# Kernel tuning notes

Measured on AMD Instinct MI355X. Metric: run time of the kernel, lower is better.

The kernel has to match this reference:

```python
import jax, jax.numpy as jnp
import numpy as np

B, T, H = 2, 2048, 1024
NH, DK = 16, 64          # num_heads, head_dim (key)
VD, DV = 1024, 64        # value_dim, head_v_dim
LCTX, CD = 512, 768      # context length, cond_token_dim
DW, DA, DG, DVR = 64, 64, 128, 16  # lora ranks: decay, a, gate, v
EPS = DK * 1e-5          # GroupNorm eps = head_dim * norm_eps
LOGW_SCALE = -0.6065306597126334   # -exp(-0.5)

def _tshift(x):
    # token shift: out[t] = x[t-1], out[0] = 0
    return jnp.pad(x, ((0, 0), (1, 0), (0, 0)))[:, :-1]

def _forward(hidden_states, context, v_first, x_r, x_w, x_k, x_v, x_a, x_g,
             k_k, k_a, r_k, W_r, W_k, W_v, W_o, W_cond,
             wA, wB, wb, aA, aB, ab, gA, gB, vA, vB, vb, gn_w, gn_b):
    b, t, _ = hidden_states.shape
    # --- cross-attention context: project then linear-resample to length t (align_corners=True) ---
    ctx = context @ W_cond                                  # [B, Lctx, H]
    L = ctx.shape[1]
    pos = jnp.arange(t) * ((L - 1) / (t - 1))
    lo = jnp.floor(pos).astype(jnp.int32)
    hi = jnp.minimum(lo + 1, L - 1)
    f = (pos - lo)[None, :, None]
    ctx = ctx[:, lo] * (1.0 - f) + ctx[:, hi] * f            # [B, T, H]

    dx = _tshift(hidden_states) - hidden_states
    dc = _tshift(ctx) - ctx
    xr = hidden_states + dx * x_r
    xw = hidden_states + dx * x_w
    xa = hidden_states + dx * x_a
    xg = hidden_states + dx * x_g
    xk = ctx + dc * x_k   # key/value come from the (resampled) context: cross attention
    xv = ctx + dc * x_v

    r = xr @ W_r
    w = LOGW_SCALE * jax.nn.sigmoid(jnp.tanh(xw @ wA) @ wB + wb)   # log decay in (-0.6065, 0)
    k = xk @ W_k
    v = xv @ W_v
    # layer_idx != 0: lerp toward v_first with learned gate
    v = v + jax.nn.sigmoid((xv @ vA) @ vB + vb) * (v_first - v)
    a = jax.nn.sigmoid((xa @ aA) @ aB + ab)                         # in-context learning rate
    g = jax.nn.sigmoid(xg @ gA) @ gB                                 # output gate (no bias)

    kk = (k * k_k).reshape(b, t, NH, DK)
    kk = kk / jnp.maximum(jnp.linalg.norm(kk, axis=-1, keepdims=True), 1e-12)
    k = k * (1.0 + (a - 1.0) * k_a)

    rh = r.reshape(b, t, NH, DK)
    wh = w.reshape(b, t, NH, DK)
    kh = k.reshape(b, t, NH, DK)
    vh = v.reshape(b, t, NH, DV)
    ah = -kk
    bh = kk * a.reshape(b, t, NH, DK)

    # --- RWKV7 generalized delta rule recurrence: S[b,h,i(val),j(key)] ---
    def step(S, inp):
        r_t, w_t, k_t, v_t, a_t, b_t = inp
        sab = jnp.einsum('bhij,bhj,bhk->bhik', S, a_t, b_t)
        S = S * jnp.exp(w_t)[:, :, None, :] + sab + jnp.einsum('bhi,bhj->bhij', v_t, k_t)
        return S, jnp.einsum('bhij,bhj->bhi', S, r_t)

    tr = lambda x: jnp.swapaxes(x, 0, 1)  # [T,B,NH,D]
    S0 = jnp.zeros((b, NH, DV, DK), hidden_states.dtype)
    _, o = jax.lax.scan(step, S0, (tr(rh), tr(wh), tr(kh), tr(vh), tr(ah), tr(bh)))
    o = jnp.swapaxes(o, 0, 1)             # [B,T,NH,DV]

    # GroupNorm(num_groups=NH) over value_dim per token
    mu = o.mean(-1, keepdims=True)
    var = o.var(-1, keepdims=True)
    o = (o - mu) * jax.lax.rsqrt(var + EPS)
    o = o.reshape(b, t, VD) * gn_w + gn_b
    # r_k-weighted direct readout
    o = o + ((rh * kh * r_k).sum(-1, keepdims=True) * vh).reshape(b, t, VD)
    return (o * g) @ W_o

def setup_inputs():
    ki = iter(jax.random.split(jax.random.key(0), 48))
    def nrm(shape, s=1.0):
        return jax.random.normal(next(ki), shape, jnp.float32) * s
    def uni(shape):
        return jax.random.uniform(next(ki), shape, dtype=jnp.float32)
    return {
        'hidden_states': nrm((B, T, H)),
        'context': nrm((B, LCTX, CD)),
        'v_first': nrm((B, T, VD)),
        'x_r': uni((1, 1, H)), 'x_w': uni((1, 1, H)), 'x_k': uni((1, 1, H)),
        'x_v': uni((1, 1, H)), 'x_a': uni((1, 1, H)), 'x_g': uni((1, 1, H)),
        'k_k': jnp.full((H,), 0.85, jnp.float32),
        'k_a': jnp.ones((H,), jnp.float32),
        'r_k': nrm((NH, DK), 0.1),
        'W_r': nrm((H, H), 0.03), 'W_k': nrm((H, H), 0.03),
        'W_v': nrm((H, VD), 0.03), 'W_o': nrm((VD, H), 0.03),
        'W_cond': nrm((CD, H), 0.03),
        'wA': nrm((H, DW), 0.05), 'wB': nrm((DW, H), 0.05), 'wb': nrm((H,), 0.3) - 4.0,
        'aA': nrm((H, DA), 0.05), 'aB': nrm((DA, H), 0.05), 'ab': nrm((H,), 0.1),
        'gA': nrm((H, DG), 0.05), 'gB': nrm((DG, VD), 0.05),
        'vA': nrm((H, DVR), 0.05), 'vB': nrm((DVR, VD), 0.05),
        'vb': jnp.ones((VD,), jnp.float32),
        'gn_w': jnp.ones((VD,), jnp.float32), 'gn_b': jnp.zeros((VD,), jnp.float32),
    }

def reference(hidden_states, context, v_first, x_r, x_w, x_k, x_v, x_a, x_g, k_k, k_a, r_k, W_r, W_k, W_v, W_o, W_cond, wA, wB, wb, aA, aB, ab, gA, gB, vA, vB, vb, gn_w, gn_b):
    return _forward(hidden_states, context, v_first, x_r, x_w, x_k, x_v, x_a, x_g, k_k, k_a, r_k, W_r, W_k, W_v, W_o, W_cond, wA, wB, wb, aA, aB, ab, gA, gB, vA, vB, vb, gn_w, gn_b)
```

## Files before the change

kernel.cpp:

```cpp
#include <hip/hip_runtime.h>
#include <cstddef>
#include <cstdint>

#define T_ 2048
#define H_ 1024
#define NH_ 16
#define LCTX 512
#define NC 64
#define CL 32

typedef __attribute__((ext_vector_type(4))) float f4;
typedef __attribute__((ext_vector_type(4))) unsigned short u16x4;
typedef __attribute__((ext_vector_type(8))) short bf16x8;
typedef __attribute__((ext_vector_type(4))) float f32x4;

#define REP16(X) X(0) X(1) X(2) X(3) X(4) X(5) X(6) X(7) X(8) X(9) X(10) X(11) X(12) X(13) X(14) X(15)
#define REP8(X) X(0) X(1) X(2) X(3) X(4) X(5) X(6) X(7)
#define REP4(X) X(0) X(1) X(2) X(3)

__device__ __forceinline__ float sgm(float x) { return 1.0f / (1.0f + expf(-x)); }
__device__ __forceinline__ f4 f4splat(float v) { f4 r; r.x = v; r.y = v; r.z = v; r.w = v; return r; }
__device__ __forceinline__ float hsum4(f4 v) { return (v.x + v.y) + (v.z + v.w); }

__device__ __forceinline__ float rdlane(float v, int l) {
    return __uint_as_float(__builtin_amdgcn_readlane(__float_as_uint(v), l));
}

__device__ __forceinline__ unsigned short f2bf(float x) {
    unsigned u = __float_as_uint(x);
    u += 0x7FFFu + ((u >> 16) & 1u);
    return (unsigned short)(u >> 16);
}
__device__ __forceinline__ float bf2f(unsigned short h) {
    return __uint_as_float(((unsigned)h) << 16);
}

__device__ __forceinline__ void split1(float x, unsigned short& h, unsigned short& l) {
    unsigned u = __float_as_uint(x);
    h = (unsigned short)(u >> 16);
    float r = x - __uint_as_float(u & 0xFFFF0000u);
    l = (unsigned short)(__float_as_uint(r) >> 16);
}
__device__ __forceinline__ void split4(f4 v, u16x4& h, u16x4& l) {
    unsigned short hh, ll;
    split1(v.x, hh, ll); h.x = hh; l.x = ll;
    split1(v.y, hh, ll); h.y = hh; l.y = ll;
    split1(v.z, hh, ll); h.z = hh; l.z = ll;
    split1(v.w, hh, ll); h.w = hh; l.w = ll;
}

__device__ __forceinline__ size_t toff4(int row, int c4, int kpan) {
    const int j = c4 & 31;
    return ((size_t)(row >> 4) * kpan + (c4 >> 5)) * 512
         + ((j & 15) >> 2) * 128 + (row & 15) * 8 + ((j >> 4) << 2);
}
__device__ __forceinline__ size_t toff1(int row, int k, int kpan) {
    const int j = k & 31;
    return ((size_t)(row >> 4) * kpan + (k >> 5)) * 512
         + ((j & 15) >> 2) * 128 + (row & 15) * 8 + ((j >> 4) << 2) + (j & 3);
}

__device__ __forceinline__ void gload16(const void* g, void* l) {
    __builtin_amdgcn_global_load_lds(
        (const __attribute__((address_space(1))) unsigned int*)g,
        (__attribute__((address_space(3))) unsigned int*)l, 16, 0, 0);
}

struct WSeg { const float* W; unsigned short* Th; unsigned short* Tl;
              int K, N, kpan, tile0, tilesN; };
struct WAll { WSeg s[13]; };

__global__ __launch_bounds__(256) void wtrans_all(WAll all)
{
    const int bid = blockIdx.x;
    int si = 0;
    #pragma unroll
    for (int i = 1; i < 13; ++i) if (bid >= all.s[i].tile0) si = i;
    const WSeg sg = all.s[si];
    const int local = bid - sg.tile0;
    const int k0 = (local / sg.tilesN) * 32;
    const int n0 = (local % sg.tilesN) * 32;

    __shared__ float tile[32][33];
    const int t = threadIdx.x;
    const int r = t >> 3, c4 = (t & 7) * 4;
    f4 v = f4splat(0.0f);
    if (k0 + r < sg.K && n0 + c4 < sg.N)
        v = *(const f4*)(sg.W + (size_t)(k0 + r) * sg.N + n0 + c4);
    tile[r][c4 + 0] = v.x; tile[r][c4 + 1] = v.y;
    tile[r][c4 + 2] = v.z; tile[r][c4 + 3] = v.w;
    __syncthreads();
    {
        const int n = n0 + r;
        float x0 = tile[c4 + 0][r], x1 = tile[c4 + 1][r];
        float x2 = tile[c4 + 2][r], x3 = tile[c4 + 3][r];
        u16x4 hv, lv;
        hv.x = f2bf(x0); lv.x = f2bf(x0 - bf2f(hv.x));
        hv.y = f2bf(x1); lv.y = f2bf(x1 - bf2f(hv.y));
        hv.z = f2bf(x2); lv.z = f2bf(x2 - bf2f(hv.z));
        hv.w = f2bf(x3); lv.w = f2bf(x3 - bf2f(hv.w));
        const size_t off = toff4(n, k0 + c4, sg.kpan);
        *(u16x4*)(sg.Th + off) = hv;
        *(u16x4*)(sg.Tl + off) = lv;
    }
}

__global__ __launch_bounds__(256) void ctx_split(
    const float* __restrict__ X, unsigned short* __restrict__ H,
    unsigned short* __restrict__ L)
{
    const int gid = blockIdx.x * 256 + threadIdx.x;
    const int row = gid / 192;
    const int c4 = (gid - row * 192) * 4;
    f4 v = *(const f4*)(X + (size_t)row * 768 + c4);
    u16x4 h, l; split4(v, h, l);
    const size_t off = toff4(row, c4, 24);
    *(u16x4*)(H + off) = h; *(u16x4*)(L + off) = l;
}

__global__ __launch_bounds__(256) void hs_lerp4(
    const float* __restrict__ hs,
    const float* __restrict__ x_r, const float* __restrict__ x_w,
    const float* __restrict__ x_a, const float* __restrict__ x_g,
    unsigned short* __restrict__ xr_h, unsigned short* __restrict__ xr_l,
    unsigned short* __restrict__ xw_h, unsigned short* __restrict__ xw_l,
    unsigned short* __restrict__ xa_h, unsigned short* __restrict__ xa_l,
    unsigned short* __restrict__ xg_h, unsigned short* __restrict__ xg_l)
{
    const int gid = blockIdx.x * 256 + threadIdx.x;
    const int c4 = (gid & 255) * 4;
    const int row = gid >> 8;
    const int tt = row & (T_ - 1);
    const f4 cur = *(const f4*)(hs + (size_t)row * H_ + c4);
    f4 prev = f4splat(0.0f);
    if (tt) prev = *(const f4*)(hs + (size_t)(row - 1) * H_ + c4);
    const f4 d = prev - cur;
    const size_t off = toff4(row, c4, 32);
    u16x4 h, l;
    split4(cur + d * (*(const f4*)(x_r + c4)), h, l);
    *(u16x4*)(xr_h + off) = h; *(u16x4*)(xr_l + off) = l;
    split4(cur + d * (*(const f4*)(x_w + c4)), h, l);
    *(u16x4*)(xw_h + off) = h; *(u16x4*)(xw_l + off) = l;
    split4(cur + d * (*(const f4*)(x_a + c4)), h, l);
    *(u16x4*)(xa_h + off) = h; *(u16x4*)(xa_l + off) = l;
    split4(cur + d * (*(const f4*)(x_g + c4)), h, l);
    *(u16x4*)(xg_h + off) = h; *(u16x4*)(xg_l + off) = l;
}

__device__ __forceinline__ f4 ctx_sample(const float* __restrict__ cp, int b, int t, int c4) {
    const float scale = (float)(511.0 / 2047.0);
    float tf = (float)t * scale;
    int lo = (int)tf;
    float f = tf - (float)lo;
    int hi = lo + 1; if (hi > LCTX - 1) hi = LCTX - 1;
    f4 cl = *(const f4*)(cp + (size_t)(b * LCTX + lo) * 1024 + c4);
    f4 ch = *(const f4*)(cp + (size_t)(b * LCTX + hi) * 1024 + c4);
    return cl + (ch - cl) * f;
}

__global__ __launch_bounds__(256) void ctx_lerp2(
    const float* __restrict__ cp,
    const float* __restrict__ x_k, const float* __restrict__ x_v,
    unsigned short* __restrict__ xk_h, unsigned short* __restrict__ xk_l,
    unsigned short* __restrict__ xv_h, unsigned short* __restrict__ xv_l)
{
    const int gid = blockIdx.x * 256 + threadIdx.x;
    const int c4 = (gid & 255) * 4;
    const int row = gid >> 8;
    const int b = row >> 11;
    const int tt = row & (T_ - 1);
    const f4 cur = ctx_sample(cp, b, tt, c4);
    f4 prev = f4splat(0.0f);
    if (tt) prev = ctx_sample(cp, b, tt - 1, c4);
    const f4 d = prev - cur;
    const size_t off = toff4(row, c4, 32);
    u16x4 h, l;
    split4(cur + d * (*(const f4*)(x_k + c4)), h, l);
    *(u16x4*)(xk_h + off) = h; *(u16x4*)(xk_l + off) = l;
    split4(cur + d * (*(const f4*)(x_v + c4)), h, l);
    *(u16x4*)(xv_h + off) = h; *(u16x4*)(xv_l + off) = l;
}

struct GSeg {
    const unsigned short* ATh; const unsigned short* ATl;
    const unsigned short* BTh; const unsigned short* BTl;
    float* C; unsigned short* Ch; unsigned short* Cl;
    const float* bias; const float* aux1; const float* aux2;
    int K, N, kpanC, epi;
};
struct GBatch { GSeg s[4]; };

template <int OSPLIT>
__global__ __launch_bounds__(256, 2) void mgemm(GBatch gb, int M)
{
    __shared__ __align__(16) unsigned short Ah_[8 * 512];
    __shared__ __align__(16) unsigned short Al_[8 * 512];
    __shared__ __align__(16) unsigned short Bh_[4 * 512];
    __shared__ __align__(16) unsigned short Bl_[4 * 512];
    const GSeg G = gb.s[blockIdx.z];
    const int bn = blockIdx.y * 64;
    if (bn >= G.N) return;
    const int K = G.K;
    const int kpan = K >> 5;
    const int tid = threadIdx.x;
    const int lane = tid & 63;
    const int wave = tid >> 6;
    const int bm = blockIdx.x * 128;
    const int g = lane >> 4, rr = lane & 15;
    const int sA0 = wave, sA1 = wave + 4;

    f32x4 acc[4][2];
    #pragma unroll
    for (int mi = 0; mi < 4; ++mi)
        #pragma unroll
        for (int ni = 0; ni < 2; ++ni)
            acc[mi][ni] = (f32x4)(0.0f);

    const size_t aBase0 = (size_t)((bm >> 4) + sA0) * kpan * 512;
    const size_t aBase1 = (size_t)((bm >> 4) + sA1) * kpan * 512;
    const size_t bBase  = (size_t)((bn >> 4) + wave) * kpan * 512;

    for (int k0 = 0; k0 < K; k0 += 32) {
        const size_t kp = (size_t)(k0 >> 5) * 512 + (size_t)lane * 8;
        gload16(G.ATh + aBase0 + kp, &Ah_[sA0 * 512]);
        gload16(G.ATh + aBase1 + kp, &Ah_[sA1 * 512]);
        gload16(G.ATl + aBase0 + kp, &Al_[sA0 * 512]);
        gload16(G.ATl + aBase1 + kp, &Al_[sA1 * 512]);
        gload16(G.BTh + bBase + kp, &Bh_[wave * 512]);
        gload16(G.BTl + bBase + kp, &Bl_[wave * 512]);
        __syncthreads();
        bf16x8 a_h[4], a_l[4], b_h[2], b_l[2];
        #pragma unroll
        for (int mi = 0; mi < 4; ++mi) {
            const int s = (wave >> 1) * 4 + mi;
            a_h[mi] = *(const bf16x8*)&Ah_[s * 512 + g * 128 + rr * 8];
            a_l[mi] = *(const bf16x8*)&Al_[s * 512 + g * 128 + rr * 8];
        }
        #pragma unroll
        for (int ni = 0; ni < 2; ++ni) {
            const int s = (wave & 1) * 2 + ni;
            b_h[ni] = *(const bf16x8*)&Bh_[s * 512 + g * 128 + rr * 8];
            b_l[ni] = *(const bf16x8*)&Bl_[s * 512 + g * 128 + rr * 8];
        }
        #pragma unroll
        for (int mi = 0; mi < 4; ++mi)
            #pragma unroll
            for (int ni = 0; ni < 2; ++ni) {
                acc[mi][ni] = __builtin_amdgcn_mfma_f32_16x16x32_bf16(a_h[mi], b_h[ni], acc[mi][ni], 0, 0, 0);
                acc[mi][ni] = __builtin_amdgcn_mfma_f32_16x16x32_bf16(a_h[mi], b_l[ni], acc[mi][ni], 0, 0, 0);
                acc[mi][ni] = __builtin_amdgcn_mfma_f32_16x16x32_bf16(a_l[mi], b_h[ni], acc[mi][ni], 0, 0, 0);
            }
        __syncthreads();
    }
    const int wm = (wave >> 1) * 64;
    const int wn = (wave & 1) * 32;
    const int epi = G.epi;
    #pragma unroll
    for (int mi = 0; mi < 4; ++mi)
        #pragma unroll
        for (int ni = 0; ni < 2; ++ni)
            #pragma unroll
            for (int q = 0; q < 4; ++q) {
                const int grow = bm + wm + mi * 16 + g * 4 + q;
                const int gcol = bn + wn + ni * 16 + rr;
                float x = acc[mi][ni][q];
                if (epi == 1) x = -0.6065306597126334f * sgm(x + G.bias[gcol]);
                else if (epi == 2) x = sgm(x + G.bias[gcol]);
                else if (epi == 3) {
                    const size_t o3 = (size_t)grow * G.N + gcol;
                    float vt = G.aux1[o3];
                    x = vt + sgm(x + G.bias[gcol]) * (G.aux2[o3] - vt);
                }
                else if (epi == 4) x = tanhf(x);
                else if (epi == 5) x = sgm(x);
                if (OSPLIT) {
                    if (gcol < G.kpanC * 32) {
                        unsigned short hh, ll;
                        split1(x, hh, ll);
                        const size_t off = toff1(grow, gcol, G.kpanC);
                        G.Ch[off] = hh; G.Cl[off] = ll;
                    }
                } else {
                    G.C[(size_t)grow * G.N + gcol] = x;
                }
            }
}

__global__ __launch_bounds__(256) void prep_k(
    float* __restrict__ k, const float* __restrict__ a,
    const float* __restrict__ k_k, const float* __restrict__ k_a,
    float* __restrict__ kk)
{
    const int gid = blockIdx.x * 256 + threadIdx.x;
    const int j = gid & 63;
    const int h = (gid >> 6) & (NH_ - 1);
    const int ch = h * 64 + j;
    const float kv = k[gid];
    float kkv = kv * k_k[ch];
    float ss = kkv * kkv;
    #pragma unroll
    for (int m = 32; m; m >>= 1) ss += __shfl_xor(ss, m, 64);
    const float nrm = fmaxf(sqrtf(ss), 1e-12f);
    kk[gid] = kkv / nrm;
    const float av = a[gid];
    k[gid] = kv * (1.0f + (av - 1.0f) * k_a[ch]);
}

__global__ __launch_bounds__(256, 1) void chunk_AU(
    const float* __restrict__ w, const float* __restrict__ k,
    const float* __restrict__ v, const float* __restrict__ kk,
    const float* __restrict__ a,
    float* __restrict__ Pbuf, float* __restrict__ Ubuf)
{
    const int bid = blockIdx.x;
    const int c = bid & (NC - 1);
    const int bh = bid >> 6;
    const int b = bh >> 4, h = bh & (NH_ - 1);
    const int tid = threadIdx.x;
    const int wv_ = tid >> 6;
    const bool isU = wv_ >= 2;
    const int lane = tid & 63;
    const int row = (wv_ & 1) * 32 + (lane >> 1);
    const int cb = (lane & 1) * 32;
    __shared__ float ew_s[2][64], ah_s[2][64], bh_s[2][64], kh_s[2][64], vh_s[2][64];

#define DECL_X(i) f4 x##i = f4splat(0.0f);
    REP8(DECL_X)
#undef DECL_X
    if (!isU) {
        const int local = row - cb;
#define INIT_Q(i) \
        if (local == 4*i+0) x##i.x = 1.0f; \
        else if (local == 4*i+1) x##i.y = 1.0f; \
        else if (local == 4*i+2) x##i.z = 1.0f; \
        else if (local == 4*i+3) x##i.w = 1.0f;
        REP8(INIT_Q)
#undef INIT_Q
    }

    size_t idx = (((size_t)b * T_ + (size_t)c * CL) * NH_ + h) * 64 + lane;
    float wvv = 0, kkv = 0, av = 0, kv = 0, vvv = 0;
    if (wv_ == 0) { wvv = w[idx]; kkv = kk[idx]; av = a[idx]; }
    else if (wv_ == 1) { kv = k[idx]; vvv = v[idx]; }
    if (wv_ == 0) { ew_s[0][lane] = expf(wvv); ah_s[0][lane] = -kkv; bh_s[0][lane] = kkv * av; }
    else if (wv_ == 1) { kh_s[0][lane] = kv; vh_s[0][lane] = vvv; }
    idx += NH_ * 64;
    if (wv_ == 0) { wvv = w[idx]; kkv = kk[idx]; av = a[idx]; }
    else if (wv_ == 1) { kv = k[idx]; vvv = v[idx]; }
    __syncthreads();

    for (int t = 0; t < CL; ++t) {
        const int buf = t & 1;
        if (t + 1 < CL) {
            const int nb = buf ^ 1;
            if (wv_ == 0) { ew_s[nb][lane] = expf(wvv); ah_s[nb][lane] = -kkv; bh_s[nb][lane] = kkv * av; }
            else if (wv_ == 1) { kh_s[nb][lane] = kv; vh_s[nb][lane] = vvv; }
            if (t + 2 < CL) {
                idx += NH_ * 64;
                if (wv_ == 0) { wvv = w[idx]; kkv = kk[idx]; av = a[idx]; }
                else if (wv_ == 1) { kv = k[idx]; vvv = v[idx]; }
            }
        }
        const f4* A4 = (const f4*)&ah_s[buf][cb];
        f4 da0 = x0 * A4[0] + x2 * A4[2];
        f4 da1 = x1 * A4[1] + x3 * A4[3];
        da0 += x4 * A4[4] + x6 * A4[6];
        da1 += x5 * A4[5] + x7 * A4[7];
        const float Dp = hsum4(da0 + da1);
        const float D = Dp + __shfl_xor(Dp, 1, 64);
        const float vcur = vh_s[buf][row];
        const f4* E4 = (const f4*)&ew_s[buf][cb];
        const f4* B4 = (const f4*)&bh_s[buf][cb];
        const f4* K4 = (const f4*)&kh_s[buf][cb];
        if (!isU) {
#define UPDQ_(i) { x##i = x##i * E4[i] + D * B4[i]; }
            REP8(UPDQ_)
#undef UPDQ_
        } else {
#define UPDU_(i) { x##i = x##i * E4[i] + D * B4[i] + vcur * K4[i]; }
            REP8(UPDU_)
#undef UPDU_
        }
        __syncthreads();
    }
    float* Dst = (isU ? Ubuf : Pbuf)
               + (((size_t)bh * NC + c) * 64 + row) * 64 + cb;
#define ST_(i) ((f4*)Dst)[i] = x##i;
    REP8(ST_)
#undef ST_
}

__global__ __launch_bounds__(64) void chunk_scan(
    const float* __restrict__ Pbuf, float* __restrict__ USbuf)
{
    const int wg = (blockIdx.x & 7) * 64 + (blockIdx.x >> 3);
    const int bh = wg >> 4;
    const int rg = wg & 15;
    const int j = threadIdx.x;
    const int r0 = rg * 4;

    float a0 = 0, a1 = 0, a2 = 0, a3 = 0;
    float u0, u1, u2, u3;
    float pA[64], pB[64];

    const size_t base = (size_t)bh * NC * 4096;
    {
        const float* Pb = Pbuf + base + j;
        #pragma unroll
        for (int k2 = 0; k2 < 64; ++k2) pA[k2] = Pb[k2 * 64];
        const float* Ub = USbuf + base + r0 * 64 + j;
        u0 = Ub[0]; u1 = Ub[64]; u2 = Ub[128]; u3 = Ub[192];
    }

#define SCAN_STEP(PC, PN, c) { \
    float n0 = u0, n1 = u1, n2 = u2, n3 = u3; \
    float* Ub = USbuf + base + (size_t)(c) * 4096 + r0 * 64 + j; \
    Ub[0] = a0; Ub[64] = a1; Ub[128] = a2; Ub[192] = a3; \
    if ((c) + 1 < NC) { \
        const float* Un = USbuf + base + (size_t)((c) + 1) * 4096 + r0 * 64 + j; \
        u0 = Un[0]; u1 = Un[64]; u2 = Un[128]; u3 = Un[192]; \
        const float* Pn = Pbuf + base + (size_t)((c) + 1) * 4096 + j; \
        _Pragma("unroll") \
        for (int k2 = 0; k2 < 64; ++k2) PN[k2] = Pn[k2 * 64]; \
    } \
    _Pragma("unroll") \
    for (int k2 = 0; k2 < 64; ++k2) { \
        const float s0 = rdlane(a0, k2), s1 = rdlane(a1, k2); \
        const float s2 = rdlane(a2, k2), s3 = rdlane(a3, k2); \
        n0 += s0 * PC[k2]; n1 += s1 * PC[k2]; \
        n2 += s2 * PC[k2]; n3 += s3 * PC[k2]; \
    } \
    a0 = n0; a1 = n1; a2 = n2; a3 = n3; }

    for (int c = 0; c < NC; c += 2) {
        SCAN_STEP(pA, pB, c)
        SCAN_STEP(pB, pA, c + 1)
    }
#undef SCAN_STEP
}

__global__ __launch_bounds__(256, 1) void chunk_out(
    const float* __restrict__ r, const float* __restrict__ w,
    const float* __restrict__ k, const float* __restrict__ v,
    const float* __restrict__ kk, const float* __restrict__ a,
    const float* __restrict__ Scbuf, float* __restrict__ o)
{
    const int bid = blockIdx.x;
    const int c = bid & (NC - 1);
    const int bh = bid >> 6;
    const int b = bh >> 4, h = bh & (NH_ - 1);
    const int tid = threadIdx.x;
    const int wv_ = tid >> 6;
    const int lane = tid & 63;
    const int row = wv_ * 16 + (lane >> 2);
    const int cb = (lane & 3) * 16;
    __shared__ float ew_s[2][64], ah_s[2][64], bh_s[2][64], kh_s[2][64], rh_s[2][64], vh_s[2][64];

#define DECL_S(i) f4 s##i;
    REP4(DECL_S)
#undef DECL_S
    const f4* Srow = (const f4*)(Scbuf + (((size_t)bh * NC + c) * 64 + row) * 64 + cb);
#define LD_S(i) s##i = Srow[i];
    REP4(LD_S)
#undef LD_S

    size_t idx = (((size_t)b * T_ + (size_t)c * CL) * NH_ + h) * 64 + lane;
    size_t obase = (((size_t)b * T_ + (size_t)c * CL) * NH_ + h) * 64;
    float wvv = 0, kkv = 0, av = 0, kv = 0, rv = 0, vvv = 0;
    if (wv_ == 0) { wvv = w[idx]; kkv = kk[idx]; av = a[idx]; }
    else if (wv_ == 1) { kv = k[idx]; rv = r[idx]; }
    else if (wv_ == 2) { vvv = v[idx]; }
    if (wv_ == 0) { ew_s[0][lane] = expf(wvv); ah_s[0][lane] = -kkv; bh_s[0][lane] = kkv * av; }
    else if (wv_ == 1) { kh_s[0][lane] = kv; rh_s[0][lane] = rv; }
    else if (wv_ == 2) { vh_s[0][lane] = vvv; }
    idx += NH_ * 64;
    if (wv_ == 0) { wvv = w[idx]; kkv = kk[idx]; av = a[idx]; }
    else if (wv_ == 1) { kv = k[idx]; rv = r[idx]; }
    else if (wv_ == 2) { vvv = v[idx]; }
    __syncthreads();

    for (int t = 0; t < CL; ++t) {
        const int buf = t & 1;
        if (t + 1 < CL) {
            const int nb = buf ^ 1;
            if (wv_ == 0) { ew_s[nb][lane] = expf(wvv); ah_s[nb][lane] = -kkv; bh_s[nb][lane] = kkv * av; }
            else if (wv_ == 1) { kh_s[nb][lane] = kv; rh_s[nb][lane] = rv; }
            else if (wv_ == 2) { vh_s[nb][lane] = vvv; }
            if (t + 2 < CL) {
                idx += NH_ * 64;
                if (wv_ == 0) { wvv = w[idx]; kkv = kk[idx]; av = a[idx]; }
                else if (wv_ == 1) { kv = k[idx]; rv = r[idx]; }
                else if (wv_ == 2) { vvv = v[idx]; }
            }
        }
        const f4* A4 = (const f4*)&ah_s[buf][cb];
        f4 ua = (s0 * A4[0] + s1 * A4[1]) + (s2 * A4[2] + s3 * A4[3]);
        float p = hsum4(ua);
        p += __shfl_xor(p, 1, 64);
        p += __shfl_xor(p, 2, 64);
        const float sa = p;
        const float vcur = vh_s[buf][row];
        const f4* E4 = (const f4*)&ew_s[buf][cb];
        const f4* B4 = (const f4*)&bh_s[buf][cb];
        const f4* K4 = (const f4*)&kh_s[buf][cb];
        const f4* R4 = (const f4*)&rh_s[buf][cb];
        f4 oa = f4splat(0.0f);
#define UPDO_(i) { s##i = s##i * E4[i] + sa * B4[i] + vcur * K4[i]; oa += s##i * R4[i]; }
        REP4(UPDO_)
#undef UPDO_
        float ow = hsum4(oa);
        ow += __shfl_xor(ow, 1, 64);
        ow += __shfl_xor(ow, 2, 64);
        if ((lane & 3) == 0) o[obase + row] = ow;
        obase += NH_ * 64;
        __syncthreads();
    }
}

__global__ __launch_bounds__(256) void postproc(
    const float* __restrict__ o, const float* __restrict__ r, const float* __restrict__ k,
    const float* __restrict__ v, const float* __restrict__ g, const float* __restrict__ r_k,
    const float* __restrict__ gn_w, const float* __restrict__ gn_b,
    unsigned short* __restrict__ og_h, unsigned short* __restrict__ og_l)
{
    const int gid = blockIdx.x * 256 + threadIdx.x;
    const int i = gid & 63;
    const int h = (gid >> 6) & (NH_ - 1);
    const int ch = h * 64 + i;
    const float ov = o[gid];
    float s1 = ov, s2 = ov * ov;
    float term = r[gid] * k[gid] * r_k[ch];
    #pragma unroll
    for (int m = 32; m; m >>= 1) {
        s1 += __shfl_xor(s1, m, 64);
        s2 += __shfl_xor(s2, m, 64);
        term += __shfl_xor(term, m, 64);
    }
    const float mu = s1 * (1.0f / 64.0f);
    const float var = s2 * (1.0f / 64.0f) - mu * mu;
    const float on = (ov - mu) * rsqrtf(var + 6.4e-4f);
    const float outv = (on * gn_w[ch] + gn_b[ch] + term * v[gid]) * g[gid];
    unsigned short hh, ll;
    split1(outv, hh, ll);
    const int row = gid >> 10;
    const int col = gid & 1023;
    const size_t off = toff1(row, col, 32);
    og_h[off] = hh; og_l[off] = ll;
}

extern "C" void kernel_launch(void* const* d_in, const int* in_sizes, int n_in,
                              void* d_out, int out_size, void* d_ws, size_t ws_size,
                              hipStream_t stream)
{
    const float* hs      = (const float*)d_in[0];
    const float* context = (const float*)d_in[1];
    const float* v_first = (const float*)d_in[2];
    const float* x_r = (const float*)d_in[3];
    const float* x_w = (const float*)d_in[4];
    const float* x_k = (const float*)d_in[5];
    const float* x_v = (const float*)d_in[6];
    const float* x_a = (const float*)d_in[7];
    const float* x_g = (const float*)d_in[8];
    const float* k_k = (const float*)d_in[9];
    const float* k_a = (const float*)d_in[10];
    const float* r_k = (const float*)d_in[11];
    const float* W_r = (const float*)d_in[12];
    const float* W_k = (const float*)d_in[13];
    const float* W_v = (const float*)d_in[14];
    const float* W_o = (const float*)d_in[15];
    const float* W_cond = (const float*)d_in[16];
    const float* wA = (const float*)d_in[17];
    const float* wB = (const float*)d_in[18];
    const float* wb = (const float*)d_in[19];
    const float* aA = (const float*)d_in[20];
    const float* aB = (const float*)d_in[21];
    const float* ab = (const float*)d_in[22];
    const float* gA = (const float*)d_in[23];
    const float* gB = (const float*)d_in[24];
    const float* vA = (const float*)d_in[25];
    const float* vB = (const float*)d_in[26];
    const float* vb = (const float*)d_in[27];
    const float* gn_w = (const float*)d_in[28];
    const float* gn_b = (const float*)d_in[29];
    (void)in_sizes; (void)n_in; (void)out_size; (void)ws_size;

    float* ws = (float*)d_ws;
    float* cp    = ws;
    float* rbuf  = cp    + (1 << 20);
    float* kbuf  = rbuf  + (4 << 20);
    float* vtmp  = kbuf  + (4 << 20);
    float* wbuf  = vtmp  + (4 << 20);
    float* abuf  = wbuf  + (4 << 20);
    float* obuf  = abuf  + (4 << 20);
    float* kkbuf = obuf  + (4 << 20);
    float* gbuf  = kkbuf + (4 << 20);
    float* vbuf  = gbuf  + (4 << 20);
    float* Pbuf  = vbuf  + (4 << 20);
    float* Ubuf  = Pbuf  + (8 << 20);
    float* endf  = Ubuf  + (8 << 20);

    unsigned short* xr_h = (unsigned short*)obuf;  unsigned short* xr_l = xr_h + (4 << 20);
    unsigned short* xw_h = (unsigned short*)Pbuf;  unsigned short* xw_l = xw_h + (4 << 20);
    unsigned short* xa_h = (unsigned short*)Ubuf;  unsigned short* xa_l = xa_h + (4 << 20);
    unsigned short* xg_h = (unsigned short*)kkbuf; unsigned short* xg_l = xg_h + (4 << 20);
    unsigned short* xk_h = (unsigned short*)gbuf;  unsigned short* xk_l = xk_h + (4 << 20);
    unsigned short* xv_h = (unsigned short*)vbuf;  unsigned short* xv_l = xv_h + (4 << 20);
    unsigned short* og_h = (unsigned short*)wbuf;  unsigned short* og_l = og_h + (4 << 20);

    unsigned short* u = (unsigned short*)endf;
    unsigned short* ctx_h = u;  u += 786432;
    unsigned short* ctx_l = u;  u += 786432;
    unsigned short* w1h = u;    u += 262144;
    unsigned short* w1l = u;    u += 262144;
    unsigned short* a1h = u;    u += 262144;
    unsigned short* a1l = u;    u += 262144;
    unsigned short* g1h = u;    u += 524288;
    unsigned short* g1l = u;    u += 524288;
    unsigned short* v1h = u;    u += 131072;
    unsigned short* v1l = u;    u += 131072;
    unsigned short* condT_h = u; u += 786432;
    unsigned short* condT_l = u; u += 786432;
    unsigned short* rT_h = u;    u += 1048576;
    unsigned short* rT_l = u;    u += 1048576;
    unsigned short* kT_h = u;    u += 1048576;
    unsigned short* kT_l = u;    u += 1048576;
    unsigned short* vT_h = u;    u += 1048576;
    unsigned short* vT_l = u;    u += 1048576;
    unsigned short* oT_h = u;    u += 1048576;
    unsigned short* oT_l = u;    u += 1048576;
    unsigned short* waT_h = u;   u += 65536;
    unsigned short* waT_l = u;   u += 65536;
    unsigned short* wbT_h = u;   u += 65536;
    unsigned short* wbT_l = u;   u += 65536;
    unsigned short* aaT_h = u;   u += 65536;
    unsigned short* aaT_l = u;   u += 65536;
    unsigned short* abT_h = u;   u += 65536;
    unsigned short* abT_l = u;   u += 65536;
    unsigned short* gaT_h = u;   u += 131072;
    unsigned short* gaT_l = u;   u += 131072;
    unsigned short* gbT_h = u;   u += 131072;
    unsigned short* gbT_l = u;   u += 131072;
    unsigned short* vaT_h = u;   u += 65536;
    unsigned short* vaT_l = u;   u += 65536;
    unsigned short* vbT_h = u;   u += 32768;
    unsigned short* vbT_l = u;   u += 32768;

    const dim3 blk(256);
    {
        WAll all;
        auto seg = [](const float* W, unsigned short* Th, unsigned short* Tl,
                      int K, int N, int Kpad, int Npad, int tile0) {
            WSeg s; s.W = W; s.Th = Th; s.Tl = Tl; s.K = K; s.N = N;
            s.kpan = Kpad / 32; s.tile0 = tile0; s.tilesN = Npad / 32; return s;
        };
        int t0 = 0;
        all.s[0]  = seg(W_cond, condT_h, condT_l, 768, 1024, 768, 1024, t0);  t0 += 24 * 32;
        all.s[1]  = seg(W_r, rT_h, rT_l, 1024, 1024, 1024, 1024, t0);         t0 += 32 * 32;
        all.s[2]  = seg(W_k, kT_h, kT_l, 1024, 1024, 1024, 1024, t0);         t0 += 32 * 32;
        all.s[3]  = seg(W_v, vT_h, vT_l, 1024, 1024, 1024, 1024, t0);         t0 += 32 * 32;
        all.s[4]  = seg(W_o, oT_h, oT_l, 1024, 1024, 1024, 1024, t0);         t0 += 32 * 32;
        all.s[5]  = seg(wA, waT_h, waT_l, 1024, 64, 1024, 64, t0);            t0 += 32 * 2;
        all.s[6]  = seg(wB, wbT_h, wbT_l, 64, 1024, 64, 1024, t0);            t0 += 2 * 32;
        all.s[7]  = seg(aA, aaT_h, aaT_l, 1024, 64, 1024, 64, t0);            t0 += 32 * 2;
        all.s[8]  = seg(aB, abT_h, abT_l, 64, 1024, 64, 1024, t0);            t0 += 2 * 32;
        all.s[9]  = seg(gA, gaT_h, gaT_l, 1024, 128, 1024, 128, t0);          t0 += 32 * 4;
        all.s[10] = seg(gB, gbT_h, gbT_l, 128, 1024, 128, 1024, t0);          t0 += 4 * 32;
        all.s[11] = seg(vA, vaT_h, vaT_l, 1024, 16, 1024, 64, t0);            t0 += 32 * 2;
        all.s[12] = seg(vB, vbT_h, vbT_l, 16, 1024, 32, 1024, t0);            t0 += 1 * 32;
        wtrans_all<<<dim3(t0), blk, 0, stream>>>(all);
    }

    auto GS = [](const unsigned short* ah, const unsigned short* al,
                 const unsigned short* bh, const unsigned short* bl,
                 float* c, unsigned short* ch, unsigned short* cl,
                 int K, int N, int kpanC, int epi,
                 const float* bias, const float* a1, const float* a2) {
        GSeg s; s.ATh = ah; s.ATl = al; s.BTh = bh; s.BTl = bl;
        s.C = c; s.Ch = ch; s.Cl = cl; s.bias = bias; s.aux1 = a1; s.aux2 = a2;
        s.K = K; s.N = N; s.kpanC = kpanC; s.epi = epi; return s;
    };

    ctx_split<<<dim3(768), blk, 0, stream>>>(context, ctx_h, ctx_l);
    hs_lerp4<<<dim3(4096), blk, 0, stream>>>(hs, x_r, x_w, x_a, x_g,
                                             xr_h, xr_l, xw_h, xw_l, xa_h, xa_l, xg_h, xg_l);
    {
        GBatch gb;
        gb.s[0] = GS(ctx_h, ctx_l, condT_h, condT_l, cp, nullptr, nullptr,
                     768, 1024, 0, 0, nullptr, nullptr, nullptr);
        gb.s[1] = gb.s[0]; gb.s[2] = gb.s[0]; gb.s[3] = gb.s[0];
        mgemm<0><<<dim3(8, 16, 1), blk, 0, stream>>>(gb, 1024);
    }
    ctx_lerp2<<<dim3(4096), blk, 0, stream>>>(cp, x_k, x_v, xk_h, xk_l, xv_h, xv_l);

    {
        GBatch gb;
        gb.s[0] = GS(xr_h, xr_l, rT_h, rT_l, rbuf, nullptr, nullptr,
                     1024, 1024, 0, 0, nullptr, nullptr, nullptr);
        gb.s[1] = GS(xk_h, xk_l, kT_h, kT_l, kbuf, nullptr, nullptr,
                     1024, 1024, 0, 0, nullptr, nullptr, nullptr);
        gb.s[2] = GS(xv_h, xv_l, vT_h, vT_l, vtmp, nullptr, nullptr,
                     1024, 1024, 0, 0, nullptr, nullptr, nullptr);
        gb.s[3] = gb.s[0];
        mgemm<0><<<dim3(32, 16, 3), blk, 0, stream>>>(gb, 4096);
    }
    {
        GBatch gb;
        gb.s[0] = GS(xw_h, xw_l, waT_h, waT_l, nullptr, w1h, w1l,
                     1024, 64, 2, 4, nullptr, nullptr, nullptr);
        gb.s[1] = GS(xa_h, xa_l, aaT_h, aaT_l, nullptr, a1h, a1l,
                     1024, 64, 2, 0, nullptr, nullptr, nullptr);
        gb.s[2] = GS(xg_h, xg_l, gaT_h, gaT_l, nullptr, g1h, g1l,
                     1024, 128, 4, 5, nullptr, nullptr, nullptr);
        gb.s[3] = GS(xv_h, xv_l, vaT_h, vaT_l, nullptr, v1h, v1l,
                     1024, 64, 1, 0, nullptr, nullptr, nullptr);
        mgemm<1><<<dim3(32, 2, 4), blk, 0, stream>>>(gb, 4096);
    }
    {
        GBatch gb;
        gb.s[0] = GS(w1h, w1l, wbT_h, wbT_l, wbuf, nullptr, nullptr,
                     64, 1024, 0, 1, wb, nullptr, nullptr);
        gb.s[1] = GS(a1h, a1l, abT_h, abT_l, abuf, nullptr, nullptr,
                     64, 1024, 0, 2, ab, nullptr, nullptr);
        gb.s[2] = GS(g1h, g1l, gbT_h, gbT_l, gbuf, nullptr, nullptr,
                     128, 1024, 0, 0, nullptr, nullptr, nullptr);
        gb.s[3] = GS(v1h, v1l, vbT_h, vbT_l, vbuf, nullptr, nullptr,
                     32, 1024, 0, 3, vb, vtmp, v_first);
        mgemm<0><<<dim3(32, 16, 4), blk, 0, stream>>>(gb, 4096);
    }

    prep_k<<<dim3(16384), blk, 0, stream>>>(kbuf, abuf, k_k, k_a, kkbuf);
    chunk_AU<<<dim3(2048), dim3(256), 0, stream>>>(wbuf, kbuf, vbuf, kkbuf, abuf, Pbuf, Ubuf);
    chunk_scan<<<dim3(512), dim3(64), 0, stream>>>(Pbuf, Ubuf);
    chunk_out<<<dim3(2048), dim3(256), 0, stream>>>(rbuf, wbuf, kbuf, vbuf, kkbuf, abuf, Ubuf, obuf);

    postproc<<<dim3(16384), blk, 0, stream>>>(obuf, rbuf, kbuf, vbuf, gbuf, r_k, gn_w, gn_b, og_h, og_l);
    {
        GBatch gb;
        gb.s[0] = GS(og_h, og_l, oT_h, oT_l, (float*)d_out, nullptr, nullptr,
                     1024, 1024, 0, 0, nullptr, nullptr, nullptr);
        gb.s[1] = gb.s[0]; gb.s[2] = gb.s[0]; gb.s[3] = gb.s[0];
        mgemm<0><<<dim3(32, 16, 1), blk, 0, stream>>>(gb, 4096);
    }
}
```

Baseline: 635.9 us.

## Map each chunk to one wavefront with per-lane state rows and readlane broadcasts

chunk_AU and chunk_out now give each (batch, head, chunk) a single 64-lane wavefront instead of a 256-thread block. Each lane holds a full 64-column state row in registers, and per-timestep vectors are broadcast with readlane instead of being staged through double-buffered shared memory behind __syncthreads. This removes the shared-memory traffic and block barriers and packs four chunks per block, so the grids shrink by four. In exchange each lane keeps 128 floats (chunk_AU) or 64 floats (chunk_out) live, which raises register pressure and can cause spills, and each step issues many readlane instructions.

```diff
diff --git a/kernel.cpp b/kernel.cpp
--- a/kernel.cpp
+++ b/kernel.cpp
@@ -13,10 +13,6 @@
 typedef __attribute__((ext_vector_type(4))) unsigned short u16x4;
 typedef __attribute__((ext_vector_type(8))) short bf16x8;
 typedef __attribute__((ext_vector_type(4))) float f32x4;
-
-#define REP16(X) X(0) X(1) X(2) X(3) X(4) X(5) X(6) X(7) X(8) X(9) X(10) X(11) X(12) X(13) X(14) X(15)
-#define REP8(X) X(0) X(1) X(2) X(3) X(4) X(5) X(6) X(7)
-#define REP4(X) X(0) X(1) X(2) X(3)
 
 __device__ __forceinline__ float sgm(float x) { return 1.0f / (1.0f + expf(-x)); }
 __device__ __forceinline__ f4 f4splat(float v) { f4 r; r.x = v; r.y = v; r.z = v; r.w = v; return r; }
@@ -306,88 +302,69 @@
     k[gid] = kv * (1.0f + (av - 1.0f) * k_a[ch]);
 }
 
-__global__ __launch_bounds__(256, 1) void chunk_AU(
+__global__ __launch_bounds__(256) void chunk_AU(
     const float* __restrict__ w, const float* __restrict__ k,
     const float* __restrict__ v, const float* __restrict__ kk,
     const float* __restrict__ a,
     float* __restrict__ Pbuf, float* __restrict__ Ubuf)
 {
-    const int bid = blockIdx.x;
-    const int c = bid & (NC - 1);
-    const int bh = bid >> 6;
+    const int gw = blockIdx.x * 4 + (threadIdx.x >> 6);
+    const int c = gw & (NC - 1);
+    const int bh = gw >> 6;
     const int b = bh >> 4, h = bh & (NH_ - 1);
-    const int tid = threadIdx.x;
-    const int wv_ = tid >> 6;
-    const bool isU = wv_ >= 2;
-    const int lane = tid & 63;
-    const int row = (wv_ & 1) * 32 + (lane >> 1);
-    const int cb = (lane & 1) * 32;
-    __shared__ float ew_s[2][64], ah_s[2][64], bh_s[2][64], kh_s[2][64], vh_s[2][64];
-
-#define DECL_X(i) f4 x##i = f4splat(0.0f);
-    REP8(DECL_X)
-#undef DECL_X
-    if (!isU) {
-        const int local = row - cb;
-#define INIT_Q(i) \
-        if (local == 4*i+0) x##i.x = 1.0f; \
-        else if (local == 4*i+1) x##i.y = 1.0f; \
-        else if (local == 4*i+2) x##i.z = 1.0f; \
-        else if (local == 4*i+3) x##i.w = 1.0f;
-        REP8(INIT_Q)
-#undef INIT_Q
-    }
+    const int lane = threadIdx.x & 63;
+
+    float q[64], uu[64];
+    #pragma unroll
+    for (int j = 0; j < 64; ++j) { q[j] = (j == lane) ? 1.0f : 0.0f; uu[j] = 0.0f; }
 
     size_t idx = (((size_t)b * T_ + (size_t)c * CL) * NH_ + h) * 64 + lane;
-    float wvv = 0, kkv = 0, av = 0, kv = 0, vvv = 0;
-    if (wv_ == 0) { wvv = w[idx]; kkv = kk[idx]; av = a[idx]; }
-    else if (wv_ == 1) { kv = k[idx]; vvv = v[idx]; }
-    if (wv_ == 0) { ew_s[0][lane] = expf(wvv); ah_s[0][lane] = -kkv; bh_s[0][lane] = kkv * av; }
-    else if (wv_ == 1) { kh_s[0][lane] = kv; vh_s[0][lane] = vvv; }
-    idx += NH_ * 64;
-    if (wv_ == 0) { wvv = w[idx]; kkv = kk[idx]; av = a[idx]; }
-    else if (wv_ == 1) { kv = k[idx]; vvv = v[idx]; }
-    __syncthreads();
+    float wv = w[idx], kkv = kk[idx], av = a[idx], kv = k[idx], vv = v[idx];
 
     for (int t = 0; t < CL; ++t) {
-        const int buf = t & 1;
+        const float e_own = expf(wv);
+        const float ah_own = -kkv;
+        const float bh_own = kkv * av;
+        const float k_own = kv;
+        const float v_own = vv;
         if (t + 1 < CL) {
-            const int nb = buf ^ 1;
-            if (wv_ == 0) { ew_s[nb][lane] = expf(wvv); ah_s[nb][lane] = -kkv; bh_s[nb][lane] = kkv * av; }
-            else if (wv_ == 1) { kh_s[nb][lane] = kv; vh_s[nb][lane] = vvv; }
-            if (t + 2 < CL) {
-                idx += NH_ * 64;
-                if (wv_ == 0) { wvv = w[idx]; kkv = kk[idx]; av = a[idx]; }
-                else if (wv_ == 1) { kv = k[idx]; vvv = v[idx]; }
-            }
+            idx += NH_ * 64;
+            wv = w[idx]; kkv = kk[idx]; av = a[idx]; kv = k[idx]; vv = v[idx];
         }
-        const f4* A4 = (const f4*)&ah_s[buf][cb];
-        f4 da0 = x0 * A4[0] + x2 * A4[2];
-        f4 da1 = x1 * A4[1] + x3 * A4[3];
-        da0 += x4 * A4[4] + x6 * A4[6];
-        da1 += x5 * A4[5] + x7 * A4[7];
-        const float Dp = hsum4(da0 + da1);
-        const float D = Dp + __shfl_xor(Dp, 1, 64);
-        const float vcur = vh_s[buf][row];
-        const f4* E4 = (const f4*)&ew_s[buf][cb];
-        const f4* B4 = (const f4*)&bh_s[buf][cb];
-        const f4* K4 = (const f4*)&kh_s[buf][cb];
-        if (!isU) {
-#define UPDQ_(i) { x##i = x##i * E4[i] + D * B4[i]; }
-            REP8(UPDQ_)
-#undef UPDQ_
-        } else {
-#define UPDU_(i) { x##i = x##i * E4[i] + D * B4[i] + vcur * K4[i]; }
-            REP8(UPDU_)
-#undef UPDU_
+        float dq0 = 0, dq1 = 0, dq2 = 0, dq3 = 0;
+        float du0 = 0, du1 = 0, du2 = 0, du3 = 0;
+        #pragma unroll
+        for (int j = 0; j < 64; j += 4) {
+            const float a0 = rdlane(ah_own, j);
+            const float a1 = rdlane(ah_own, j + 1);
+            const float a2 = rdlane(ah_own, j + 2);
+            const float a3 = rdlane(ah_own, j + 3);
+            dq0 += q[j] * a0;     dq1 += q[j + 1] * a1;
+            dq2 += q[j + 2] * a2; dq3 += q[j + 3] * a3;
+            du0 += uu[j] * a0;     du1 += uu[j + 1] * a1;
+            du2 += uu[j + 2] * a2; du3 += uu[j + 3] * a3;
         }
-        __syncthreads();
-    }
-    float* Dst = (isU ? Ubuf : Pbuf)
-               + (((size_t)bh * NC + c) * 64 + row) * 64 + cb;
-#define ST_(i) ((f4*)Dst)[i] = x##i;
-    REP8(ST_)
-#undef ST_
+        const float Dq = (dq0 + dq1) + (dq2 + dq3);
+        const float Du = (du0 + du1) + (du2 + du3);
+        #pragma unroll
+        for (int j = 0; j < 64; ++j) {
+            const float ej = rdlane(e_own, j);
+            const float bj = rdlane(bh_own, j);
+            const float kj = rdlane(k_own, j);
+            q[j]  = q[j]  * ej + Dq * bj;
+            uu[j] = uu[j] * ej + Du * bj + v_own * kj;
+        }
+    }
+    float* Pd = Pbuf + (((size_t)bh * NC + c) * 64 + lane) * 64;
+    float* Ud = Ubuf + (((size_t)bh * NC + c) * 64 + lane) * 64;
+    #pragma unroll
+    for (int jj = 0; jj < 16; ++jj) {
+        f4 tp, tu;
+        tp.x = q[4 * jj];  tp.y = q[4 * jj + 1];  tp.z = q[4 * jj + 2];  tp.w = q[4 * jj + 3];
+        tu.x = uu[4 * jj]; tu.y = uu[4 * jj + 1]; tu.z = uu[4 * jj + 2]; tu.w = uu[4 * jj + 3];
+        *(f4*)(Pd + 4 * jj) = tp;
+        *(f4*)(Ud + 4 * jj) = tu;
+    }
 }
 
 __global__ __launch_bounds__(64) void chunk_scan(
@@ -439,81 +416,75 @@
 #undef SCAN_STEP
 }
 
-__global__ __launch_bounds__(256, 1) void chunk_out(
+__global__ __launch_bounds__(256) void chunk_out(
     const float* __restrict__ r, const float* __restrict__ w,
     const float* __restrict__ k, const float* __restrict__ v,
     const float* __restrict__ kk, const float* __restrict__ a,
     const float* __restrict__ Scbuf, float* __restrict__ o)
 {
-    const int bid = blockIdx.x;
-    const int c = bid & (NC - 1);
-    const int bh = bid >> 6;
+    const int gw = blockIdx.x * 4 + (threadIdx.x >> 6);
+    const int c = gw & (NC - 1);
+    const int bh = gw >> 6;
     const int b = bh >> 4, h = bh & (NH_ - 1);
-    const int tid = threadIdx.x;
-    const int wv_ = tid >> 6;
-    const int lane = tid & 63;
-    const int row = wv_ * 16 + (lane >> 2);
-    const int cb = (lane & 3) * 16;
-    __shared__ float ew_s[2][64], ah_s[2][64], bh_s[2][64], kh_s[2][64], rh_s[2][64], vh_s[2][64];
-
-#define DECL_S(i) f4 s##i;
-    REP4(DECL_S)
-#undef DECL_S
-    const f4* Srow = (const f4*)(Scbuf + (((size_t)bh * NC + c) * 64 + row) * 64 + cb);
-#define LD_S(i) s##i = Srow[i];
-    REP4(LD_S)
-#undef LD_S
+    const int lane = threadIdx.x & 63;
+
+    float s[64];
+    {
+        const float* Srow = Scbuf + (((size_t)bh * NC + c) * 64 + lane) * 64;
+        #pragma unroll
+        for (int j = 0; j < 64; ++j) s[j] = Srow[j];
+    }
 
     size_t idx = (((size_t)b * T_ + (size_t)c * CL) * NH_ + h) * 64 + lane;
     size_t obase = (((size_t)b * T_ + (size_t)c * CL) * NH_ + h) * 64;
-    float wvv = 0, kkv = 0, av = 0, kv = 0, rv = 0, vvv = 0;
-    if (wv_ == 0) { wvv = w[idx]; kkv = kk[idx]; av = a[idx]; }
-    else if (wv_ == 1) { kv = k[idx]; rv = r[idx]; }
-    else if (wv_ == 2) { vvv = v[idx]; }
-    if (wv_ == 0) { ew_s[0][lane] = expf(wvv); ah_s[0][lane] = -kkv; bh_s[0][lane] = kkv * av; }
-    else if (wv_ == 1) { kh_s[0][lane] = kv; rh_s[0][lane] = rv; }
-    else if (wv_ == 2) { vh_s[0][lane] = vvv; }
-    idx += NH_ * 64;
-    if (wv_ == 0) { wvv = w[idx]; kkv = kk[idx]; av = a[idx]; }
-    else if (wv_ == 1) { kv = k[idx]; rv = r[idx]; }
-    else if (wv_ == 2) { vvv = v[idx]; }
-    __syncthreads();
+    float wv = w[idx], kkv = kk[idx], av = a[idx], kv = k[idx], rv = r[idx], vv = v[idx];
 
     for (int t = 0; t < CL; ++t) {
-        const int buf = t & 1;
+        const float e_own = expf(wv);
+        const float ah_own = -kkv;
+        const float bh_own = kkv * av;
+        const float k_own = kv;
+        const float r_own = rv;
+        const float v_own = vv;
         if (t + 1 < CL) {
-            const int nb = buf ^ 1;
-            if (wv_ == 0) { ew_s[nb][lane] = expf(wvv); ah_s[nb][lane] = -kkv; bh_s[nb][lane] = kkv * av; }
-            else if (wv_ == 1) { kh_s[nb][lane] = kv; rh_s[nb][lane] = rv; }
-            else if (wv_ == 2) { vh_s[nb][lane] = vvv; }
-            if (t + 2 < CL) {
-                idx += NH_ * 64;
-                if (wv_ == 0) { wvv = w[idx]; kkv = kk[idx]; av = a[idx]; }
-                else if (wv_ == 1) { kv = k[idx]; rv = r[idx]; }
-                else if (wv_ == 2) { vvv = v[idx]; }
+            idx += NH_ * 64;
+            wv = w[idx]; kkv = kk[idx]; av = a[idx]; kv = k[idx]; rv = r[idx]; vv = v[idx];
+        }
+        float d0 = 0, d1 = 0, d2 = 0, d3 = 0;
+        #pragma unroll
+        for (int j = 0; j < 64; j += 4) {
+            d0 += s[j]     * rdlane(ah_own, j);
+            d1 += s[j + 1] * rdlane(ah_own, j + 1);
+            d2 += s[j + 2] * rdlane(ah_own, j + 2);
+            d3 += s[j + 3] * rdlane(ah_own, j + 3);
+        }
+        const float sa = (d0 + d1) + (d2 + d3);
+        float o0 = 0, o1 = 0, o2 = 0, o3 = 0;
+        #pragma unroll
+        for (int j = 0; j < 64; j += 4) {
+            {
+                const float ej = rdlane(e_own, j), bj = rdlane(bh_own, j);
+                const float kj = rdlane(k_own, j), rj = rdlane(r_own, j);
+                s[j] = s[j] * ej + sa * bj + v_own * kj; o0 += s[j] * rj;
+            }
+            {
+                const float ej = rdlane(e_own, j + 1), bj = rdlane(bh_own, j + 1);
+                const float kj = rdlane(k_own, j + 1), rj = rdlane(r_own, j + 1);
+                s[j + 1] = s[j + 1] * ej + sa * bj + v_own * kj; o1 += s[j + 1] * rj;
+            }
+            {
+                const float ej = rdlane(e_own, j + 2), bj = rdlane(bh_own, j + 2);
+                const float kj = rdlane(k_own, j + 2), rj = rdlane(r_own, j + 2);
+                s[j + 2] = s[j + 2] * ej + sa * bj + v_own * kj; o2 += s[j + 2] * rj;
+            }
+            {
+                const float ej = rdlane(e_own, j + 3), bj = rdlane(bh_own, j + 3);
+                const float kj = rdlane(k_own, j + 3), rj = rdlane(r_own, j + 3);
+                s[j + 3] = s[j + 3] * ej + sa * bj + v_own * kj; o3 += s[j + 3] * rj;
             }
         }
-        const f4* A4 = (const f4*)&ah_s[buf][cb];
-        f4 ua = (s0 * A4[0] + s1 * A4[1]) + (s2 * A4[2] + s3 * A4[3]);
-        float p = hsum4(ua);
-        p += __shfl_xor(p, 1, 64);
-        p += __shfl_xor(p, 2, 64);
-        const float sa = p;
-        const float vcur = vh_s[buf][row];
-        const f4* E4 = (const f4*)&ew_s[buf][cb];
-        const f4* B4 = (const f4*)&bh_s[buf][cb];
-        const f4* K4 = (const f4*)&kh_s[buf][cb];
-        const f4* R4 = (const f4*)&rh_s[buf][cb];
-        f4 oa = f4splat(0.0f);
-#define UPDO_(i) { s##i = s##i * E4[i] + sa * B4[i] + vcur * K4[i]; oa += s##i * R4[i]; }
-        REP4(UPDO_)
-#undef UPDO_
-        float ow = hsum4(oa);
-        ow += __shfl_xor(ow, 1, 64);
-        ow += __shfl_xor(ow, 2, 64);
-        if ((lane & 3) == 0) o[obase + row] = ow;
+        o[obase + lane] = (o0 + o1) + (o2 + o3);
         obase += NH_ * 64;
-        __syncthreads();
     }
 }
 
@@ -729,9 +700,9 @@
     }
 
     prep_k<<<dim3(16384), blk, 0, stream>>>(kbuf, abuf, k_k, k_a, kkbuf);
-    chunk_AU<<<dim3(2048), dim3(256), 0, stream>>>(wbuf, kbuf, vbuf, kkbuf, abuf, Pbuf, Ubuf);
+    chunk_AU<<<dim3(512), dim3(256), 0, stream>>>(wbuf, kbuf, vbuf, kkbuf, abuf, Pbuf, Ubuf);
     chunk_scan<<<dim3(512), dim3(64), 0, stream>>>(Pbuf, Ubuf);
-    chunk_out<<<dim3(2048), dim3(256), 0, stream>>>(rbuf, wbuf, kbuf, vbuf, kkbuf, abuf, Ubuf, obuf);
+    chunk_out<<<dim3(512), dim3(256), 0, stream>>>(rbuf, wbuf, kbuf, vbuf, kkbuf, abuf, Ubuf, obuf);
 
     postproc<<<dim3(16384), blk, 0, stream>>>(obuf, rbuf, kbuf, vbuf, gbuf, r_k, gn_w, gn_b, og_h, og_l);
     {
```

After: 642.8 us. About the same (+1.1%).
